# Optimization experiments

Measured on AMD Instinct MI355X. Metric: run time of the kernel, lower is better.

Reference implementation:

```python
import jax, jax.numpy as jnp
import numpy as np
import math

N_HEAD = 32
N_HEAD_KV = 8
HEAD_DIM = 64
ROTARY_DIM = 32  # partial rotary: applied to first ROTARY_DIM dims of each head
ROPE_BASE = 10000.0


def setup_inputs() -> dict:
    key = jax.random.key(0)
    ks = jax.random.split(key, 5)
    B, S, D = 1, 2048, N_HEAD * HEAD_DIM
    qkv_dim = (N_HEAD + 2 * N_HEAD_KV) * HEAD_DIM
    scale = 1.0 / math.sqrt(D)
    return {
        "x": jax.random.normal(ks[0], (B, S, D), dtype=jnp.float32),
        "Wqkv": jax.random.normal(ks[1], (D, qkv_dim), dtype=jnp.float32) * scale,
        "bqkv": jax.random.normal(ks[2], (qkv_dim,), dtype=jnp.float32) * 0.01,
        "Wout": jax.random.normal(ks[3], (D, D), dtype=jnp.float32) * scale,
        "bout": jax.random.normal(ks[4], (D,), dtype=jnp.float32) * 0.01,
    }


def _rope_cos_sin(seqlen):
    # inv_freq over half the rotary dims, positions in fp32 (pos_idx_in_fp32=True)
    inv_freq = 1.0 / (ROPE_BASE ** (jnp.arange(0, ROTARY_DIM, 2, dtype=jnp.float32) / ROTARY_DIM))
    t = jnp.arange(seqlen, dtype=jnp.float32)
    freqs = jnp.outer(t, inv_freq)  # [S, ROTARY_DIM//2]
    return jnp.cos(freqs), jnp.sin(freqs)


def _apply_rotary(x, cos, sin):
    # x: [B, S, H, head_dim]; rotate first ROTARY_DIM dims, pass the rest
    x_rot, x_pass = x[..., :ROTARY_DIM], x[..., ROTARY_DIM:]
    x1, x2 = jnp.split(x_rot, 2, axis=-1)
    c = cos[None, :, None, :]  # broadcast over batch and heads
    s = sin[None, :, None, :]
    x_rot = jnp.concatenate([x1 * c - x2 * s, x1 * s + x2 * c], axis=-1)
    return jnp.concatenate([x_rot.astype(x.dtype), x_pass], axis=-1)


def reference(x, Wqkv, bqkv, Wout, bout):
    B, S, D = x.shape
    # fused QKV projection
    qkv = x @ Wqkv + bqkv  # [B, S, (H + 2*Hkv) * hd]
    q = qkv[..., : N_HEAD * HEAD_DIM].reshape(B, S, N_HEAD, HEAD_DIM)
    kv = qkv[..., N_HEAD * HEAD_DIM :].reshape(B, S, 2, N_HEAD_KV, HEAD_DIM)

    cos, sin = _rope_cos_sin(S)
    q = _apply_rotary(q, cos, sin)
    k = _apply_rotary(kv[:, :, 0], cos, sin)  # rotary on K only (as in _apply_rotary_emb_kv)
    v = kv[:, :, 1]

    # GQA: repeat kv heads g times contiguously -> (hkv g)
    g = N_HEAD // N_HEAD_KV
    k = jnp.repeat(k, g, axis=2)  # [B, S, H, hd]
    v = jnp.repeat(v, g, axis=2)

    softmax_scale = 1.0 / math.sqrt(HEAD_DIM)
    scores = jnp.einsum("bthd,bshd->bhts", q.astype(jnp.float32), k.astype(jnp.float32) * softmax_scale)

    # causal mask with -10000 (matches torch masked_fill), seqlen_q == seqlen_k
    rows = jnp.arange(S)[:, None]
    cols = jnp.arange(S)[None, :]
    causal_mask = cols > rows  # [S, S]
    scores = jnp.where(causal_mask[None, None], jnp.float32(-10000.0), scores)

    attention = jax.nn.softmax(scores, axis=-1).astype(v.dtype)
    out = jnp.einsum("bhts,bshd->bthd", attention, v)  # [B, S, H, hd]
    out = out.reshape(B, S, N_HEAD * HEAD_DIM)
    return out @ Wout + bout
```

## Files before the change

### kernel.cpp

```cpp
#include <hip/hip_runtime.h>

typedef unsigned short ushort_t;
typedef __attribute__((ext_vector_type(8))) __bf16 bf16x8;
typedef __attribute__((ext_vector_type(4))) float f32x4;
typedef __attribute__((ext_vector_type(8))) unsigned short ushort8;
typedef __attribute__((ext_vector_type(4))) int int4v;

constexpr int S = 2048;
constexpr int D = 2048;
constexpr int NQKV = 3072;
constexpr int NH = 32, DH = 64;

static __device__ __forceinline__ float bf2f(ushort_t u) {
    return __uint_as_float(((unsigned int)u) << 16);
}
static __device__ __forceinline__ ushort_t f2bf(float f) {
    unsigned int u = __float_as_uint(f);
    u = (u + 0x7fffu + ((u >> 16) & 1u)) >> 16;
    return (ushort_t)u;
}

#define GLD16(gp, sp)                                                          \
    __builtin_amdgcn_global_load_lds(                                          \
        (const __attribute__((address_space(1))) void*)(gp),                   \
        (__attribute__((address_space(3))) void*)(sp), 16, 0, 0)

__global__ void k_cvt(const float* __restrict__ src, ushort_t* __restrict__ dst, int n4) {
    int i = blockIdx.x * blockDim.x + threadIdx.x;
    if (i < n4) {
        float4 v = ((const float4*)src)[i];
        ushort4 o;
        o.x = f2bf(v.x); o.y = f2bf(v.y); o.z = f2bf(v.z); o.w = f2bf(v.w);
        ((ushort4*)dst)[i] = o;
    }
}

__global__ void k_transpose_cvt(const float* __restrict__ src, ushort_t* __restrict__ dst,
                                int R, int C) {
    __shared__ float tile[32][33];
    int c0 = blockIdx.x * 32, r0 = blockIdx.y * 32;
    int tx = threadIdx.x, ty = threadIdx.y;
#pragma unroll
    for (int j = 0; j < 32; j += 8)
        tile[ty + j][tx] = src[(size_t)(r0 + ty + j) * C + c0 + tx];
    __syncthreads();
#pragma unroll
    for (int j = 0; j < 32; j += 8)
        dst[(size_t)(c0 + ty + j) * R + r0 + tx] = f2bf(tile[tx][ty + j]);
}

template <bool OUT_F32>
__global__ __launch_bounds__(256) void k_gemm(
    const ushort_t* __restrict__ A,
    const ushort_t* __restrict__ BT,
    const float* __restrict__ bias,
    void* __restrict__ Cout,
    int M, int N, int K)
{
    constexpr int BK = 32;
    __shared__ ushort_t As[2][128 * BK];
    __shared__ ushort_t Bs[2][128 * BK];
    const int m0 = blockIdx.y * 128;
    const int n0 = blockIdx.x * 128;
    const int t = threadIdx.x;
    const int lane = t & 63, wid = t >> 6;
    const int wm = (wid >> 1) * 64, wn = (wid & 1) * 64;
    const int lr = lane & 15, kg = (lane >> 4) * 8;

    const int srow = lane >> 2;
    const int scol = (lane & 3) * 8;
    const ushort_t* gA = A + (size_t)(m0 + wid * 32 + srow) * K + scol;
    const ushort_t* gB = BT + (size_t)(n0 + wid * 32 + srow) * K + scol;
    const int lofs = (wid * 32) * BK;

#define STAGE(buf, kk)                                                         \
    do {                                                                       \
        GLD16(gA + (kk), &As[buf][lofs]);                                      \
        GLD16(gA + (size_t)16 * K + (kk), &As[buf][lofs + 16 * BK]);           \
        GLD16(gB + (kk), &Bs[buf][lofs]);                                      \
        GLD16(gB + (size_t)16 * K + (kk), &Bs[buf][lofs + 16 * BK]);           \
    } while (0)

    f32x4 acc[4][4] = {};

    STAGE(0, 0);
    asm volatile("s_waitcnt vmcnt(0)");
    __syncthreads();

    int cur = 0;
    for (int k0 = 0; k0 < K; k0 += BK) {
        if (k0 + BK < K) STAGE(cur ^ 1, k0 + BK);
        bf16x8 af[4], bfr[4];
#pragma unroll
        for (int i = 0; i < 4; ++i) {
            af[i]  = *(const bf16x8*)&As[cur][(wm + i * 16 + lr) * BK + kg];
            bfr[i] = *(const bf16x8*)&Bs[cur][(wn + i * 16 + lr) * BK + kg];
        }
#pragma unroll
        for (int i = 0; i < 4; ++i)
#pragma unroll
            for (int j = 0; j < 4; ++j)
                acc[i][j] = __builtin_amdgcn_mfma_f32_16x16x32_bf16(af[i], bfr[j], acc[i][j], 0, 0, 0);
        asm volatile("s_waitcnt vmcnt(0)");
        __syncthreads();
        cur ^= 1;
    }
#undef STAGE

    const int lg = (lane >> 4) * 4;
#pragma unroll
    for (int j = 0; j < 4; ++j) {
        int n = n0 + wn + j * 16 + lr;
        float bv = bias[n];
#pragma unroll
        for (int i = 0; i < 4; ++i) {
#pragma unroll
            for (int r = 0; r < 4; ++r) {
                int m = m0 + wm + i * 16 + lg + r;
                float v = acc[i][j][r] + bv;
                if constexpr (OUT_F32) ((float*)Cout)[(size_t)m * N + n] = v;
                else ((ushort_t*)Cout)[(size_t)m * N + n] = f2bf(v);
            }
        }
    }
}

__global__ void k_rope(ushort_t* qkv) {
    int idx = blockIdx.x * blockDim.x + threadIdx.x;
    int i = idx & 15;
    int sh = idx >> 4;
    int h = sh % 40;
    int s = sh / 40;
    if (s >= S) return;
    int col = (h < 32) ? h * 64 : 2048 + (h - 32) * 64;
    ushort_t* p = qkv + (size_t)s * NQKV + col;
    float x1 = bf2f(p[i]), x2 = bf2f(p[i + 16]);
    float inv = exp2f(-(float)i * 0.83048202372f);
    float f = (float)s * inv;
    float c, sn;
    sincosf(f, &sn, &c);
    p[i]      = f2bf(x1 * c - x2 * sn);
    p[i + 16] = f2bf(x1 * sn + x2 * c);
}

__global__ __launch_bounds__(512) void k_attn(const ushort_t* __restrict__ qkv,
                                              ushort_t* __restrict__ out) {
    __shared__ ushort_t Ks[64 * 72];
    __shared__ ushort_t Vs[64 * 64];

    const int h = blockIdx.x;
    const int by = blockIdx.y;
    const int qb = (by < 8) ? by : 23 - by;
    const int q0 = qb * 128;
    const int kvh = h >> 2;
    const int t = threadIdx.x, lane = t & 63, w = t >> 6;
    const int lr = lane & 15, g = lane >> 4;
    const int qw = q0 + w * 16;
    const int qg = qw + lr;

    bf16x8 qf0, qf1;
    {
        const ushort_t* qp = qkv + (size_t)qg * NQKV + h * DH + g * 8;
        qf0 = *(const bf16x8*)&qp[0];
        qf1 = *(const bf16x8*)&qp[32];
    }
    const int idx0 = (lr + 16 * (2 * (g & 1))) << 2;
    const int idx1 = (lr + 16 * (2 * (g & 1) + 1)) << 2;
    const bool hi = (g >> 1) != 0;

    float mrun = -1e30f, lrun = 0.f;
    f32x4 o[4] = {};

    const int sr = t >> 3, sc = (t & 7) * 8;
    const ushort_t* gK = qkv + (size_t)sr * NQKV + 2048 + kvh * DH + sc;
    const ushort_t* gV = qkv + (size_t)sr * NQKV + 2560 + kvh * DH + sc;

    const int ntile = (q0 + 128) / 64;
    for (int kt = 0; kt < ntile; ++kt) {
        const int kv0 = kt * 64;
        {
            ushort8 kk = *(const ushort8*)&gK[(size_t)kv0 * NQKV];
            *(ushort8*)&Ks[sr * 72 + sc] = kk;
            ushort8 vv = *(const ushort8*)&gV[(size_t)kv0 * NQKV];
#pragma unroll
            for (int e = 0; e < 8; ++e) Vs[(sc + e) * 64 + (sr ^ sc)] = vv[e];
        }
        __syncthreads();
        if (kv0 <= qw) {
            f32x4 s[4];
#pragma unroll
            for (int nt = 0; nt < 4; ++nt) {
                bf16x8 a0 = *(const bf16x8*)&Ks[(nt * 16 + lr) * 72 + g * 8];
                bf16x8 a1 = *(const bf16x8*)&Ks[(nt * 16 + lr) * 72 + 32 + g * 8];
                f32x4 a = {};
                a = __builtin_amdgcn_mfma_f32_16x16x32_bf16(a0, qf0, a, 0, 0, 0);
                a = __builtin_amdgcn_mfma_f32_16x16x32_bf16(a1, qf1, a, 0, 0, 0);
                s[nt] = a;
            }
            float tmax = -3e38f;
#pragma unroll
            for (int nt = 0; nt < 4; ++nt)
#pragma unroll
                for (int r = 0; r < 4; ++r) {
                    float v = s[nt][r] * 0.125f;
                    int kvg = kv0 + nt * 16 + 4 * g + r;
                    v = (kvg > qg) ? -1e30f : v;
                    s[nt][r] = v;
                    tmax = fmaxf(tmax, v);
                }
            tmax = fmaxf(tmax, __shfl_xor(tmax, 16));
            tmax = fmaxf(tmax, __shfl_xor(tmax, 32));
            float mn = fmaxf(mrun, tmax);
            float alpha = __expf(mrun - mn);
            float sum = 0.f;
#pragma unroll
            for (int nt = 0; nt < 4; ++nt)
#pragma unroll
                for (int r = 0; r < 4; ++r) {
                    float p = __expf(s[nt][r] - mn);
                    s[nt][r] = p;
                    sum += p;
                }
            sum += __shfl_xor(sum, 16);
            sum += __shfl_xor(sum, 32);
            lrun = lrun * alpha + sum;
            mrun = mn;
#pragma unroll
            for (int tt = 0; tt < 4; ++tt) o[tt] *= alpha;

            int pk[8];
#pragma unroll
            for (int nt = 0; nt < 4; ++nt)
#pragma unroll
                for (int rp = 0; rp < 2; ++rp) {
                    int dd;
                    asm("v_cvt_pk_bf16_f32 %0, %1, %2"
                        : "=v"(dd) : "v"(s[nt][2 * rp]), "v"(s[nt][2 * rp + 1]));
                    pk[nt * 2 + rp] = dd;
                }
#pragma unroll
            for (int ks = 0; ks < 2; ++ks) {
                int a0 = __builtin_amdgcn_ds_bpermute(idx0, pk[(2 * ks) * 2 + 0]);
                int b0 = __builtin_amdgcn_ds_bpermute(idx0, pk[(2 * ks + 1) * 2 + 0]);
                int a1 = __builtin_amdgcn_ds_bpermute(idx0, pk[(2 * ks) * 2 + 1]);
                int b1 = __builtin_amdgcn_ds_bpermute(idx0, pk[(2 * ks + 1) * 2 + 1]);
                int a2 = __builtin_amdgcn_ds_bpermute(idx1, pk[(2 * ks) * 2 + 0]);
                int b2 = __builtin_amdgcn_ds_bpermute(idx1, pk[(2 * ks + 1) * 2 + 0]);
                int a3 = __builtin_amdgcn_ds_bpermute(idx1, pk[(2 * ks) * 2 + 1]);
                int b3 = __builtin_amdgcn_ds_bpermute(idx1, pk[(2 * ks + 1) * 2 + 1]);
                int4v pb;
                pb.x = hi ? b0 : a0;
                pb.y = hi ? b1 : a1;
                pb.z = hi ? b2 : a2;
                pb.w = hi ? b3 : a3;
                bf16x8 pf = __builtin_bit_cast(bf16x8, pb);
#pragma unroll
                for (int tt = 0; tt < 4; ++tt) {
                    const int dh = tt * 16 + lr;
                    bf16x8 va = *(const bf16x8*)&Vs[dh * 64 + ((32 * ks + g * 8) ^ (dh & 56))];
                    o[tt] = __builtin_amdgcn_mfma_f32_16x16x32_bf16(va, pf, o[tt], 0, 0, 0);
                }
            }
        }
        __syncthreads();
    }
    float inv = 1.0f / lrun;
    ushort_t* op = out + (size_t)qg * D + h * DH;
#pragma unroll
    for (int tt = 0; tt < 4; ++tt) {
#pragma unroll
        for (int rp = 0; rp < 2; ++rp) {
            int dd;
            float va = o[tt][2 * rp] * inv, vb = o[tt][2 * rp + 1] * inv;
            asm("v_cvt_pk_bf16_f32 %0, %1, %2" : "=v"(dd) : "v"(va), "v"(vb));
            *(int*)&op[tt * 16 + 4 * g + 2 * rp] = dd;
        }
    }
}

extern "C" void kernel_launch(void* const* d_in, const int* in_sizes, int n_in,
                              void* d_out, int out_size, void* d_ws, size_t ws_size,
                              hipStream_t stream) {
    const float* x    = (const float*)d_in[0];
    const float* Wqkv = (const float*)d_in[1];
    const float* bqkv = (const float*)d_in[2];
    const float* Wout = (const float*)d_in[3];
    const float* bout = (const float*)d_in[4];
    float* out = (float*)d_out;

    char* ws = (char*)d_ws;
    ushort_t* xb    = (ushort_t*)(ws);
    ushort_t* wqkvT = (ushort_t*)(ws + (8u  << 20));
    ushort_t* woutT = (ushort_t*)(ws + (20u << 20));
    ushort_t* qkvb  = (ushort_t*)(ws + (28u << 20));
    ushort_t* ao    = (ushort_t*)(ws + (40u << 20));

    k_cvt<<<(S * D / 4 + 255) / 256, 256, 0, stream>>>(x, xb, S * D / 4);
    k_transpose_cvt<<<dim3(NQKV / 32, D / 32), dim3(32, 8), 0, stream>>>(Wqkv, wqkvT, D, NQKV);
    k_transpose_cvt<<<dim3(D / 32, D / 32), dim3(32, 8), 0, stream>>>(Wout, woutT, D, D);
    k_gemm<false><<<dim3(NQKV / 128, S / 128), 256, 0, stream>>>(xb, wqkvT, bqkv, qkvb, S, NQKV, D);
    k_rope<<<(S * 40 * 16) / 256, 256, 0, stream>>>(qkvb);
    k_attn<<<dim3(NH, 16), 512, 0, stream>>>(qkvb, ao);
    k_gemm<true><<<dim3(D / 128, S / 128), 256, 0, stream>>>(ao, woutT, bout, out, S, D, D);
}
```

Before: 272.2 us.

## Triple-buffer GEMM LDS staging and prefetch next K/V tile in attention

The GEMM main loop moves from double to triple buffering of the A/B LDS tiles. Two tiles stay in flight, with partial vmcnt waits and raw s_barrier in place of waiting for all loads each iteration. The attention kernel now loads the next K/V tile into registers right after the barrier, so global latency overlaps the QK/softmax/PV compute. The cost is more LDS per GEMM block, which may reduce occupancy, and extra registers held across the attention loop.

```diff
diff --git a/kernel.cpp b/kernel.cpp
--- a/kernel.cpp
+++ b/kernel.cpp
@@ -58,8 +58,8 @@
     int M, int N, int K)
 {
     constexpr int BK = 32;
-    __shared__ ushort_t As[2][128 * BK];
-    __shared__ ushort_t Bs[2][128 * BK];
+    __shared__ ushort_t As[3][128 * BK];
+    __shared__ ushort_t Bs[3][128 * BK];
     const int m0 = blockIdx.y * 128;
     const int n0 = blockIdx.x * 128;
     const int t = threadIdx.x;
@@ -81,31 +81,49 @@
         GLD16(gB + (size_t)16 * K + (kk), &Bs[buf][lofs + 16 * BK]);           \
     } while (0)
 
+#define COMPUTE(bufi)                                                          \
+    do {                                                                       \
+        bf16x8 af[4], bfr[4];                                                  \
+        _Pragma("unroll")                                                      \
+        for (int i = 0; i < 4; ++i) {                                          \
+            af[i]  = *(const bf16x8*)&As[bufi][(wm + i * 16 + lr) * BK + kg];  \
+            bfr[i] = *(const bf16x8*)&Bs[bufi][(wn + i * 16 + lr) * BK + kg];  \
+        }                                                                      \
+        _Pragma("unroll")                                                      \
+        for (int i = 0; i < 4; ++i)                                            \
+            _Pragma("unroll")                                                  \
+            for (int j = 0; j < 4; ++j)                                        \
+                acc[i][j] = __builtin_amdgcn_mfma_f32_16x16x32_bf16(           \
+                    af[i], bfr[j], acc[i][j], 0, 0, 0);                        \
+    } while (0)
+
     f32x4 acc[4][4] = {};
+    const int NK = K / BK;
 
     STAGE(0, 0);
-    asm volatile("s_waitcnt vmcnt(0)");
-    __syncthreads();
-
+    STAGE(1, BK);
     int cur = 0;
-    for (int k0 = 0; k0 < K; k0 += BK) {
-        if (k0 + BK < K) STAGE(cur ^ 1, k0 + BK);
-        bf16x8 af[4], bfr[4];
-#pragma unroll
-        for (int i = 0; i < 4; ++i) {
-            af[i]  = *(const bf16x8*)&As[cur][(wm + i * 16 + lr) * BK + kg];
-            bfr[i] = *(const bf16x8*)&Bs[cur][(wn + i * 16 + lr) * BK + kg];
-        }
-#pragma unroll
-        for (int i = 0; i < 4; ++i)
-#pragma unroll
-            for (int j = 0; j < 4; ++j)
-                acc[i][j] = __builtin_amdgcn_mfma_f32_16x16x32_bf16(af[i], bfr[j], acc[i][j], 0, 0, 0);
-        asm volatile("s_waitcnt vmcnt(0)");
-        __syncthreads();
-        cur ^= 1;
-    }
+    for (int i = 0; i < NK - 2; ++i) {
+        int nbuf = cur + 2; if (nbuf >= 3) nbuf -= 3;
+        STAGE(nbuf, (i + 2) * BK);
+        asm volatile("s_waitcnt vmcnt(8)" ::: "memory");
+        __builtin_amdgcn_s_barrier();
+        COMPUTE(cur);
+        asm volatile("" ::: "memory");
+        __builtin_amdgcn_s_barrier();
+        ++cur; if (cur == 3) cur = 0;
+    }
+    asm volatile("s_waitcnt vmcnt(4)" ::: "memory");
+    __builtin_amdgcn_s_barrier();
+    COMPUTE(cur);
+    asm volatile("" ::: "memory");
+    __builtin_amdgcn_s_barrier();
+    ++cur; if (cur == 3) cur = 0;
+    asm volatile("s_waitcnt vmcnt(0)" ::: "memory");
+    __builtin_amdgcn_s_barrier();
+    COMPUTE(cur);
 #undef STAGE
+#undef COMPUTE
 
     const int lg = (lane >> 4) * 4;
 #pragma unroll
@@ -176,16 +194,20 @@
     const ushort_t* gV = qkv + (size_t)sr * NQKV + 2560 + kvh * DH + sc;
 
     const int ntile = (q0 + 128) / 64;
+    ushort8 kk = *(const ushort8*)&gK[0];
+    ushort8 vv = *(const ushort8*)&gV[0];
     for (int kt = 0; kt < ntile; ++kt) {
         const int kv0 = kt * 64;
         {
-            ushort8 kk = *(const ushort8*)&gK[(size_t)kv0 * NQKV];
             *(ushort8*)&Ks[sr * 72 + sc] = kk;
-            ushort8 vv = *(const ushort8*)&gV[(size_t)kv0 * NQKV];
 #pragma unroll
             for (int e = 0; e < 8; ++e) Vs[(sc + e) * 64 + (sr ^ sc)] = vv[e];
         }
         __syncthreads();
+        if (kt + 1 < ntile) {
+            kk = *(const ushort8*)&gK[(size_t)(kv0 + 64) * NQKV];
+            vv = *(const ushort8*)&gV[(size_t)(kv0 + 64) * NQKV];
+        }
         if (kv0 <= qw) {
             f32x4 s[4];
 #pragma unroll
```

Result: faster. 264.1 us (-3.0%).
